# Performance work log

Hardware: AMD Instinct MI355X
Metric: run time of the kernel (lower is better)

## Reference

```python
import jax, jax.numpy as jnp
import numpy as np

N, E, F_IN, H, C = 50000, 800000, 256, 64, 40
NEG_SLOPE = 0.2


def setup_inputs() -> dict:
    key = jax.random.key(0)
    ks = jax.random.split(key, 16)
    sc = lambda fan: 1.0 / np.sqrt(fan)
    return {
        "x": jax.random.normal(ks[0], (N, F_IN), dtype=jnp.float32),
        "edge_index": jax.random.randint(ks[1], (2, E), 0, N, dtype=jnp.int64),
        "W1l": jax.random.normal(ks[2], (F_IN, H), dtype=jnp.float32) * sc(F_IN),
        "b1l": jnp.zeros((H,), jnp.float32),
        "W1r": jax.random.normal(ks[3], (F_IN, H), dtype=jnp.float32) * sc(F_IN),
        "b1r": jnp.zeros((H,), jnp.float32),
        "att1": jax.random.normal(ks[4], (H,), dtype=jnp.float32) * sc(H),
        "bias1": jnp.zeros((H,), jnp.float32),
        "lin1_W": jax.random.normal(ks[5], (F_IN, H), dtype=jnp.float32) * sc(F_IN),
        "lin1_b": jnp.zeros((H,), jnp.float32),
        "W2l": jax.random.normal(ks[6], (H, C), dtype=jnp.float32) * sc(H),
        "b2l": jnp.zeros((C,), jnp.float32),
        "W2r": jax.random.normal(ks[7], (H, C), dtype=jnp.float32) * sc(H),
        "b2r": jnp.zeros((C,), jnp.float32),
        "att2": jax.random.normal(ks[8], (C,), dtype=jnp.float32) * sc(C),
        "bias2": jnp.zeros((C,), jnp.float32),
        "lin2_W": jax.random.normal(ks[9], (H, C), dtype=jnp.float32) * sc(H),
        "lin2_b": jnp.zeros((C,), jnp.float32),
    }


def gatv2_layer(x, src, dst, Wl, bl, Wr, br, att, bias, n):
    # PyG GATv2Conv, heads=1: xl = lin_l(x) (source), xr = lin_r(x) (target)
    xl = x @ Wl + bl                               # [n, out]
    xr = x @ Wr + br                               # [n, out]
    m = xl[src] + xr[dst]                          # [E, out] per-edge gather
    e = jax.nn.leaky_relu(m, NEG_SLOPE) @ att      # [E] attention logits
    # segment softmax over destination nodes (self-loops guarantee nonempty segments)
    emax = jax.ops.segment_max(e, dst, num_segments=n)
    ee = jnp.exp(e - emax[dst])
    denom = jax.ops.segment_sum(ee, dst, num_segments=n)
    alpha = ee / denom[dst]                        # [E]
    out = jax.ops.segment_sum(alpha[:, None] * xl[src], dst, num_segments=n)
    return out + bias


def reference(x, edge_index, W1l, b1l, W1r, b1r, att1, bias1, lin1_W, lin1_b,
              W2l, b2l, W2r, b2r, att2, bias2, lin2_W, lin2_b):
    n = x.shape[0]
    loops = jnp.arange(n, dtype=edge_index.dtype)
    src = jnp.concatenate([edge_index[0], loops])  # add_self_loops=True (PyG default)
    dst = jnp.concatenate([edge_index[1], loops])
    h = jax.nn.relu(gatv2_layer(x, src, dst, W1l, b1l, W1r, b1r, att1, bias1, n)
                    + x @ lin1_W + lin1_b)
    o = (gatv2_layer(h, src, dst, W2l, b2l, W2r, b2r, att2, bias2, n)
         + h @ lin2_W + lin2_b)
    return jax.nn.log_softmax(o, axis=1), edge_index
```

## Files before the change

### kernel.cpp

```cpp
#include <hip/hip_runtime.h>
#include <cmath>

#define NN 50000
#define NP 50048
#define NE 800000
#define CD 40
#define NEG_SLOPE 0.2f
#define NITEMS (NE + NN)
#define CHUNK 2048
#define NCH 416
#define NBKT 391
#define BCAP 3072
#define GB1 782
#define TB1 (3 * 64 * 256)
#define TB2 (3 * 64 * 64)
#define WPB 240

typedef __attribute__((ext_vector_type(8))) short s16x8;
typedef __attribute__((ext_vector_type(4))) float f32x4;
typedef __attribute__((ext_vector_type(2))) float f32x2;

__device__ __forceinline__ f32x2 pk_fma(f32x2 a, f32x2 b, f32x2 c) {
#if __has_builtin(__builtin_elementwise_fma)
  return __builtin_elementwise_fma(a, b, c);
#else
  f32x2 r; r[0] = fmaf(a[0], b[0], c[0]); r[1] = fmaf(a[1], b[1], c[1]); return r;
#endif
}
__device__ __forceinline__ f32x2 pk_max(f32x2 a, f32x2 b) {
#if __has_builtin(__builtin_elementwise_max)
  return __builtin_elementwise_max(a, b);
#else
  f32x2 r; r[0] = fmaxf(a[0], b[0]); r[1] = fmaxf(a[1], b[1]); return r;
#endif
}

__device__ __forceinline__ short f2bf(float x) {
  unsigned u = __builtin_bit_cast(unsigned, x);
  u += 0x7fffu + ((u >> 16) & 1u);
  return (short)(u >> 16);
}
__device__ __forceinline__ unsigned pack2(float lo, float hi) {
  return (unsigned)(unsigned short)f2bf(lo) | ((unsigned)(unsigned short)f2bf(hi) << 16);
}
__device__ __forceinline__ float bf2f_lo(unsigned v) {
  return __builtin_bit_cast(float, v << 16);
}
__device__ __forceinline__ float bf2f_hi(unsigned v) {
  return __builtin_bit_cast(float, v & 0xffff0000u);
}
__device__ __forceinline__ void unp8(uint4 v, f32x2* f) {
  f[0] = (f32x2){bf2f_lo(v.x), bf2f_hi(v.x)};
  f[1] = (f32x2){bf2f_lo(v.y), bf2f_hi(v.y)};
  f[2] = (f32x2){bf2f_lo(v.z), bf2f_hi(v.z)};
  f[3] = (f32x2){bf2f_lo(v.w), bf2f_hi(v.w)};
}

__global__ __launch_bounds__(256) void prep_bin(const float* __restrict__ W1l,
                                                const float* __restrict__ W1r,
                                                const float* __restrict__ L1,
                                                const float* __restrict__ W2l,
                                                const float* __restrict__ W2r,
                                                const float* __restrict__ L2,
                                                short* __restrict__ Wp1,
                                                short* __restrict__ Wp2,
                                                const int* __restrict__ ei,
                                                float* __restrict__ outE,
                                                int* __restrict__ gcur,
                                                unsigned* __restrict__ rec) {
  const int tid = threadIdx.x;
  if (blockIdx.x < WPB) {
    int e = blockIdx.x * 256 + tid;
    if (e < TB1) {
      int kb = e / 6144, r = e % 6144;
      int w = r / 2048, r2 = r % 2048;
      int t = r2 / 512, r3 = r2 % 512;
      int lane = r3 / 8, j = r3 % 8;
      int n = t * 16 + (lane & 15);
      int k = kb * 32 + (lane >> 4) * 8 + j;
      const float* W = (w == 0) ? W1l : (w == 1) ? W1r : L1;
      Wp1[e] = f2bf(W[k * 64 + n]);
    } else {
      e -= TB1;
      int kb = e / 6144, r = e % 6144;
      int w = r / 2048, r2 = r % 2048;
      int t = r2 / 512, r3 = r2 % 512;
      int lane = r3 / 8, j = r3 % 8;
      int n = t * 16 + (lane & 15);
      int k = kb * 32 + (lane >> 4) * 8 + j;
      const float* W = (w == 0) ? W2l : (w == 1) ? W2r : L2;
      Wp2[e] = (n < 40) ? f2bf(W[k * 40 + n]) : (short)0;
    }
    return;
  }
  __shared__ unsigned sorted[CHUNK];
  __shared__ int hist[512];
  __shared__ int bcur[512];
  __shared__ int gbase[512];
  const int base = (blockIdx.x - WPB) * CHUNK;
  for (int t = tid; t < 512; t += 256) { hist[t] = 0; bcur[t] = 0; gbase[t] = 0; }
  __syncthreads();
  unsigned key[CHUNK / 256];
#pragma unroll
  for (int u = 0; u < CHUNK / 256; ++u) {
    const int j = base + u * 256 + tid;
    unsigned k = 0xFFFFFFFFu;
    if (j < NITEMS) {
      int s, d;
      if (j < NE) {
        s = ei[j]; d = ei[NE + j];
        outE[j] = (float)s; outE[NE + j] = (float)d;
      } else {
        s = j - NE; d = s;
      }
      k = ((unsigned)d << 16) | (unsigned)s;
      atomicAdd(&hist[k >> 23], 1);
    }
    key[u] = k;
  }
  __syncthreads();
  if (tid < 64) {
    int carry = 0;
#pragma unroll
    for (int c = 0; c < 8; ++c) {
      int v = hist[c * 64 + tid];
      int inc = v;
#pragma unroll
      for (int off = 1; off < 64; off <<= 1) {
        int tt = __shfl_up(inc, off, 64);
        if (tid >= off) inc += tt;
      }
      hist[c * 64 + tid] = carry + inc - v;
      carry += __shfl(inc, 63, 64);
    }
  }
  __syncthreads();
#pragma unroll
  for (int u = 0; u < CHUNK / 256; ++u) {
    const unsigned k = key[u];
    if (k != 0xFFFFFFFFu) {
      const int b = k >> 23;
      sorted[hist[b] + atomicAdd(&bcur[b], 1)] = k;
    }
  }
  __syncthreads();
  for (int t = tid; t < NBKT; t += 256) {
    const int c = bcur[t];
    if (c > 0) gbase[t] = atomicAdd(&gcur[t], c);
  }
  __syncthreads();
  const int cnt = min(CHUNK, NITEMS - base);
  for (int i = tid; i < cnt; i += 256) {
    const unsigned k = sorted[i];
    const int b = k >> 23;
    const int p = gbase[b] + (i - hist[b]);
    if (p < BCAP) rec[(size_t)b * BCAP + p] = k;
  }
}

__device__ __forceinline__ void gemm1_body(int bid, const float* __restrict__ X,
                                           const short* __restrict__ Wp,
                                           const float* __restrict__ B0,
                                           const float* __restrict__ B1,
                                           const float* __restrict__ B2,
                                           unsigned short* __restrict__ Y0,
                                           unsigned short* __restrict__ Y1,
                                           unsigned short* __restrict__ Y2) {
  const int lane = threadIdx.x & 63;
  const int wave = threadIdx.x >> 6;
  const int r0 = bid * 64 + wave * 16;
  const int m = lane & 15;
  const int q = lane >> 4;
  f32x4 acc[3][4] = {};
  const float* a0 = X + (size_t)min(r0 + m, NN - 1) * 256 + q * 8;
  const short* bp = Wp + lane * 8;
  float4 v0 = *reinterpret_cast<const float4*>(a0);
  float4 v1 = *reinterpret_cast<const float4*>(a0 + 4);
#pragma unroll
  for (int kb = 0; kb < 8; ++kb) {
    s16x8 bf[12];
#pragma unroll
    for (int i = 0; i < 12; ++i)
      bf[i] = *reinterpret_cast<const s16x8*>(bp + (size_t)(kb * 12 + i) * 512);
    s16x8 af;
    af[0] = f2bf(v0.x); af[1] = f2bf(v0.y); af[2] = f2bf(v0.z); af[3] = f2bf(v0.w);
    af[4] = f2bf(v1.x); af[5] = f2bf(v1.y); af[6] = f2bf(v1.z); af[7] = f2bf(v1.w);
    if (kb < 7) {
      v0 = *reinterpret_cast<const float4*>(a0 + (kb + 1) * 32);
      v1 = *reinterpret_cast<const float4*>(a0 + (kb + 1) * 32 + 4);
    }
#pragma unroll
    for (int i = 0; i < 12; ++i)
      acc[i >> 2][i & 3] = __builtin_amdgcn_mfma_f32_16x16x32_bf16(
          af, bf[i], acc[i >> 2][i & 3], 0, 0, 0);
  }
#pragma unroll
  for (int w = 0; w < 3; ++w) {
    const float* B = (w == 0) ? B0 : (w == 1) ? B1 : B2;
    unsigned short* Y = (w == 0) ? Y0 : (w == 1) ? Y1 : Y2;
#pragma unroll
    for (int t = 0; t < 4; ++t) {
      const int c = t * 16 + m;
      const float bv = B[c];
#pragma unroll
      for (int rg = 0; rg < 4; ++rg) {
        const int row = r0 + q * 4 + rg;
        if (row < NN)
          Y[(size_t)row * 64 + c] = (unsigned short)f2bf(acc[w][t][rg] + bv);
      }
    }
  }
}

__global__ __launch_bounds__(256, 2) void build_gemm1(
    const float* __restrict__ X, const short* __restrict__ Wp1,
    const float* __restrict__ B0, const float* __restrict__ B1,
    const float* __restrict__ B2, unsigned short* __restrict__ Y0,
    unsigned short* __restrict__ Y1, unsigned short* __restrict__ Y2,
    const int* __restrict__ gcur, const unsigned* __restrict__ rec,
    int* __restrict__ offsets, unsigned short* __restrict__ csr16) {
  if (blockIdx.x < GB1) {
    gemm1_body(blockIdx.x, X, Wp1, B0, B1, B2, Y0, Y1, Y2);
    return;
  }
  const int b = blockIdx.x - GB1;
  const int tid = threadIdx.x;
  __shared__ unsigned recs[BCAP];
  __shared__ int red[256];
  __shared__ int cnt[128];
  __shared__ int sc[128];
  __shared__ int cur[128];
  int acc = 0;
  for (int t = tid; t < NBKT; t += 256)
    if (t < b) acc += gcur[t];
  red[tid] = acc;
  __syncthreads();
#pragma unroll
  for (int off = 128; off >= 1; off >>= 1) {
    if (tid < off) red[tid] += red[tid + off];
    __syncthreads();
  }
  const int base = red[0];
  const int Tb = min(gcur[b], BCAP);
  if (tid < 128) cnt[tid] = 0;
  __syncthreads();
  for (int i = tid; i < Tb; i += 256) {
    const unsigned k = rec[(size_t)b * BCAP + i];
    recs[i] = k;
    atomicAdd(&cnt[(k >> 16) & 127], 1);
  }
  __syncthreads();
  if (tid < 128) sc[tid] = cnt[tid];
  __syncthreads();
#pragma unroll
  for (int off = 1; off < 128; off <<= 1) {
    int v = (tid < 128 && tid >= off) ? sc[tid - off] : 0;
    __syncthreads();
    if (tid < 128) sc[tid] += v;
    __syncthreads();
  }
  if (tid < 128) {
    const int n = b * 128 + tid;
    if (n < NN) offsets[n + 1] = base + sc[tid];
    cur[tid] = sc[tid] - cnt[tid];
  }
  if (b == 0 && tid == 0) offsets[0] = 0;
  __syncthreads();
  for (int i = tid; i < Tb; i += 256) {
    const unsigned k = recs[i];
    const int p = atomicAdd(&cur[(k >> 16) & 127], 1);
    csr16[base + p] = (unsigned short)(k & 0xFFFFu);
  }
}

__global__ __launch_bounds__(256, 2) void gemm2(const short* __restrict__ Xb,
                                                const short* __restrict__ Wp,
                                                const float* __restrict__ B0,
                                                const float* __restrict__ B1,
                                                const float* __restrict__ B2,
                                                unsigned short* __restrict__ Y0,
                                                unsigned short* __restrict__ Y1,
                                                unsigned short* __restrict__ Y2) {
  const int lane = threadIdx.x & 63;
  const int wave = threadIdx.x >> 6;
  const int r0 = blockIdx.x * 64 + wave * 16;
  const int m = lane & 15;
  const int q = lane >> 4;
  f32x4 acc[3][4] = {};
  const short* a0 = Xb + (size_t)(r0 + m) * 64 + q * 8;
  const short* bp = Wp + lane * 8;
#pragma unroll
  for (int kb = 0; kb < 2; ++kb) {
    s16x8 bf[12];
#pragma unroll
    for (int i = 0; i < 12; ++i)
      bf[i] = *reinterpret_cast<const s16x8*>(bp + (size_t)(kb * 12 + i) * 512);
    const s16x8 af = *reinterpret_cast<const s16x8*>(a0 + kb * 32);
#pragma unroll
    for (int i = 0; i < 12; ++i)
      acc[i >> 2][i & 3] = __builtin_amdgcn_mfma_f32_16x16x32_bf16(
          af, bf[i], acc[i >> 2][i & 3], 0, 0, 0);
  }
#pragma unroll
  for (int w = 0; w < 3; ++w) {
    const float* B = (w == 0) ? B0 : (w == 1) ? B1 : B2;
    unsigned short* Y = (w == 0) ? Y0 : (w == 1) ? Y1 : Y2;
#pragma unroll
    for (int t = 0; t < 4; ++t) {
      const int c = t * 16 + m;
      const float bv = (c < 40) ? B[c] : 0.f;
#pragma unroll
      for (int rg = 0; rg < 4; ++rg) {
        const int row = r0 + q * 4 + rg;
        if (row < NN)
          Y[(size_t)row * 64 + c] = (unsigned short)f2bf(acc[w][t][rg] + bv);
      }
    }
  }
}

template <int OC, bool FINAL>
__global__ __launch_bounds__(256) void gat_agg(const unsigned short* __restrict__ XL,
                                               const unsigned short* __restrict__ XR,
                                               const unsigned short* __restrict__ XLIN,
                                               const float* __restrict__ att,
                                               const float* __restrict__ bias,
                                               const int* __restrict__ offsets,
                                               const unsigned short* __restrict__ csr,
                                               float* __restrict__ out,
                                               unsigned short* __restrict__ outb) {
  const int lane = threadIdx.x & 63;
  const int g = lane >> 3;
  const int l = lane & 7;
  const int d = blockIdx.x * 4 + (threadIdx.x >> 6);
  if (d >= NN) return;
  const bool dimok = (8 * l < OC);
  f32x2 a2[4] = {};
  if (dimok) {
    const float4 t0 = *reinterpret_cast<const float4*>(&att[8 * l]);
    const float4 t1 = *reinterpret_cast<const float4*>(&att[8 * l + 4]);
    a2[0] = (f32x2){t0.x, t0.y}; a2[1] = (f32x2){t0.z, t0.w};
    a2[2] = (f32x2){t1.x, t1.y}; a2[3] = (f32x2){t1.z, t1.w};
  }
  f32x2 xr2[4];
  unp8(*reinterpret_cast<const uint4*>(XR + (size_t)d * 64 + 8 * l), xr2);
  const int beg = offsets[d];
  const int end = offsets[d + 1];
  float D = 0.f;
  f32x2 A2[4] = {};
  const f32x2 ns = (f32x2){NEG_SLOPE, NEG_SLOPE};
  const int nit = (end - beg + 7) >> 3;
  const int i0 = beg + g;
  int sa = (int)csr[(i0 < end) ? i0 : beg];
  uint4 raw_next = *reinterpret_cast<const uint4*>(XL + (size_t)sa * 64 + 8 * l);
  const int i1 = i0 + 8;
  sa = (int)csr[(i1 < end) ? i1 : beg];
  for (int it = 0; it < nit; ++it) {
    const uint4 raw = raw_next;
    const bool act = (beg + it * 8 + g) < end;
    raw_next = *reinterpret_cast<const uint4*>(XL + (size_t)sa * 64 + 8 * l);
    const int i2 = beg + (it + 2) * 8 + g;
    sa = (int)csr[(i2 < end) ? i2 : beg];
    f32x2 xl2[4];
    unp8(raw, xl2);
    f32x2 pacc = (f32x2){0.f, 0.f};
#pragma unroll
    for (int j = 0; j < 4; ++j) {
      const f32x2 t = xl2[j] + xr2[j];
      const f32x2 lr = pk_max(t, t * ns);
      pacc = pk_fma(lr, a2[j], pacc);
    }
    float p = pacc[0] + pacc[1];
    p += __shfl_xor(p, 1, 64);
    p += __shfl_xor(p, 2, 64);
    p += __shfl_xor(p, 4, 64);
    const float w = __expf(act ? p : -INFINITY);
    D += w;
    const f32x2 w2 = (f32x2){w, w};
#pragma unroll
    for (int j = 0; j < 4; ++j) A2[j] = pk_fma(w2, xl2[j], A2[j]);
  }
  D += __shfl_xor(D, 8, 64);
  D += __shfl_xor(D, 16, 64);
  D += __shfl_xor(D, 32, 64);
  float A[8];
#pragma unroll
  for (int j = 0; j < 4; ++j) {
#pragma unroll
    for (int c = 0; c < 2; ++c) {
      float v = A2[j][c];
      v += __shfl_xor(v, 8, 64);
      v += __shfl_xor(v, 16, 64);
      v += __shfl_xor(v, 32, 64);
      A[j * 2 + c] = v;
    }
  }
  f32x2 xlin2[4];
  unp8(*reinterpret_cast<const uint4*>(XLIN + (size_t)d * 64 + 8 * l), xlin2);
  float b[8] = {};
  if (dimok) {
    const float4 t0 = *reinterpret_cast<const float4*>(&bias[8 * l]);
    const float4 t1 = *reinterpret_cast<const float4*>(&bias[8 * l + 4]);
    b[0] = t0.x; b[1] = t0.y; b[2] = t0.z; b[3] = t0.w;
    b[4] = t1.x; b[5] = t1.y; b[6] = t1.z; b[7] = t1.w;
  }
  const float inv = 1.0f / D;
  float val[8];
#pragma unroll
  for (int j = 0; j < 8; ++j)
    val[j] = fmaf(A[j], inv, b[j]) + xlin2[j >> 1][j & 1];
  if (!FINAL) {
    if (g == 0) {
      uint4 o;
      o.x = pack2(fmaxf(val[0], 0.f), fmaxf(val[1], 0.f));
      o.y = pack2(fmaxf(val[2], 0.f), fmaxf(val[3], 0.f));
      o.z = pack2(fmaxf(val[4], 0.f), fmaxf(val[5], 0.f));
      o.w = pack2(fmaxf(val[6], 0.f), fmaxf(val[7], 0.f));
      *reinterpret_cast<uint4*>(&outb[(size_t)d * 64 + 8 * l]) = o;
    }
  } else {
    float mx = -3e38f;
    if (dimok) {
#pragma unroll
      for (int j = 0; j < 8; ++j) mx = fmaxf(mx, val[j]);
    }
    mx = fmaxf(mx, __shfl_xor(mx, 1, 64));
    mx = fmaxf(mx, __shfl_xor(mx, 2, 64));
    mx = fmaxf(mx, __shfl_xor(mx, 4, 64));
    float es = 0.f;
    if (dimok) {
#pragma unroll
      for (int j = 0; j < 8; ++j) es += __expf(val[j] - mx);
    }
    es += __shfl_xor(es, 1, 64);
    es += __shfl_xor(es, 2, 64);
    es += __shfl_xor(es, 4, 64);
    const float lse = mx + __logf(es);
    if (g == 0 && dimok) {
      float4 o0, o1;
      o0.x = val[0] - lse; o0.y = val[1] - lse; o0.z = val[2] - lse; o0.w = val[3] - lse;
      o1.x = val[4] - lse; o1.y = val[5] - lse; o1.z = val[6] - lse; o1.w = val[7] - lse;
      float* dst = &out[(size_t)d * OC + 8 * l];
      *reinterpret_cast<float4*>(dst) = o0;
      *reinterpret_cast<float4*>(dst + 4) = o1;
    }
  }
}

extern "C" void kernel_launch(void* const* d_in, const int* in_sizes, int n_in,
                              void* d_out, int out_size, void* d_ws, size_t ws_size,
                              hipStream_t stream) {
  const float* x     = (const float*)d_in[0];
  const int*   ei    = (const int*)d_in[1];
  const float* W1l   = (const float*)d_in[2];
  const float* b1l   = (const float*)d_in[3];
  const float* W1r   = (const float*)d_in[4];
  const float* b1r   = (const float*)d_in[5];
  const float* att1  = (const float*)d_in[6];
  const float* bias1 = (const float*)d_in[7];
  const float* lin1W = (const float*)d_in[8];
  const float* lin1b = (const float*)d_in[9];
  const float* W2l   = (const float*)d_in[10];
  const float* b2l   = (const float*)d_in[11];
  const float* W2r   = (const float*)d_in[12];
  const float* b2r   = (const float*)d_in[13];
  const float* att2  = (const float*)d_in[14];
  const float* bias2 = (const float*)d_in[15];
  const float* lin2W = (const float*)d_in[16];
  const float* lin2b = (const float*)d_in[17];
  float* out = (float*)d_out;

  char* ws = (char*)d_ws;
  size_t off = 0;
  auto alloc = [&](size_t bytes) -> void* {
    void* p = ws + off;
    off += (bytes + 255) & ~(size_t)255;
    return p;
  };
  short* Wp1 = (short*)alloc((size_t)TB1 * 2);
  short* Wp2 = (short*)alloc((size_t)TB2 * 2);
  unsigned short* XL1   = (unsigned short*)alloc((size_t)NN * 64 * 2);
  unsigned short* XR1   = (unsigned short*)alloc((size_t)NN * 64 * 2);
  unsigned short* XLIN1 = (unsigned short*)alloc((size_t)NN * 64 * 2);
  unsigned short* Hb    = (unsigned short*)alloc((size_t)NP * 64 * 2);
  unsigned short* XL2   = (unsigned short*)alloc((size_t)NN * 64 * 2);
  unsigned short* XR2   = (unsigned short*)alloc((size_t)NN * 64 * 2);
  unsigned short* XLIN2 = (unsigned short*)alloc((size_t)NN * 64 * 2);
  int* gcur    = (int*)alloc((size_t)NBKT * 4);
  int* offsets = (int*)alloc((size_t)(NN + 1) * 4);
  unsigned* rec = (unsigned*)alloc((size_t)NBKT * BCAP * 4);
  unsigned short* csr = (unsigned short*)alloc((size_t)NITEMS * 2);

  hipMemsetAsync(gcur, 0, (size_t)NBKT * 4, stream);
  prep_bin<<<WPB + NCH, 256, 0, stream>>>(W1l, W1r, lin1W, W2l, W2r, lin2W,
                                          Wp1, Wp2, ei, out + (size_t)NN * CD,
                                          gcur, rec);
  build_gemm1<<<GB1 + NBKT, 256, 0, stream>>>(x, Wp1, b1l, b1r, lin1b,
                                              XL1, XR1, XLIN1, gcur, rec,
                                              offsets, csr);
  gat_agg<64, false><<<(NN + 3) / 4, 256, 0, stream>>>(XL1, XR1, XLIN1, att1,
                                                       bias1, offsets, csr,
                                                       nullptr, Hb);
  gemm2<<<GB1, 256, 0, stream>>>((const short*)Hb, Wp2, b2l, b2r, lin2b,
                                 XL2, XR2, XLIN2);
  gat_agg<40, true><<<(NN + 3) / 4, 256, 0, stream>>>(XL2, XR2, XLIN2, att2,
                                                      bias2, offsets, csr,
                                                      out, nullptr);
}
```

Baseline: 234.4 us.

## Fuse layer-1 aggregation with layer-2 GEMM through shared memory

Merges the first GATv2 aggregation kernel and the second-layer projection GEMM into one 1024-thread kernel. Each block aggregates 16 destination nodes (one per wave), writes the ReLU'd hidden rows to LDS, then 12 waves each run two MFMA ops to produce the XL2/XR2/XLIN2 tiles. This removes one launch and the global write and read of the hidden activation H. In exchange, the MFMA tail leaves four waves idle, and the barrier makes the whole block wait for its slowest node's edge loop.

After: 255.5 us. +9.0%, slower.

```diff
diff --git a/kernel.cpp b/kernel.cpp
--- a/kernel.cpp
+++ b/kernel.cpp
@@ -273,70 +273,23 @@
   }
 }
 
-__global__ __launch_bounds__(256, 2) void gemm2(const short* __restrict__ Xb,
-                                                const short* __restrict__ Wp,
-                                                const float* __restrict__ B0,
-                                                const float* __restrict__ B1,
-                                                const float* __restrict__ B2,
-                                                unsigned short* __restrict__ Y0,
-                                                unsigned short* __restrict__ Y1,
-                                                unsigned short* __restrict__ Y2) {
-  const int lane = threadIdx.x & 63;
-  const int wave = threadIdx.x >> 6;
-  const int r0 = blockIdx.x * 64 + wave * 16;
-  const int m = lane & 15;
-  const int q = lane >> 4;
-  f32x4 acc[3][4] = {};
-  const short* a0 = Xb + (size_t)(r0 + m) * 64 + q * 8;
-  const short* bp = Wp + lane * 8;
-#pragma unroll
-  for (int kb = 0; kb < 2; ++kb) {
-    s16x8 bf[12];
-#pragma unroll
-    for (int i = 0; i < 12; ++i)
-      bf[i] = *reinterpret_cast<const s16x8*>(bp + (size_t)(kb * 12 + i) * 512);
-    const s16x8 af = *reinterpret_cast<const s16x8*>(a0 + kb * 32);
-#pragma unroll
-    for (int i = 0; i < 12; ++i)
-      acc[i >> 2][i & 3] = __builtin_amdgcn_mfma_f32_16x16x32_bf16(
-          af, bf[i], acc[i >> 2][i & 3], 0, 0, 0);
-  }
-#pragma unroll
-  for (int w = 0; w < 3; ++w) {
-    const float* B = (w == 0) ? B0 : (w == 1) ? B1 : B2;
-    unsigned short* Y = (w == 0) ? Y0 : (w == 1) ? Y1 : Y2;
-#pragma unroll
-    for (int t = 0; t < 4; ++t) {
-      const int c = t * 16 + m;
-      const float bv = (c < 40) ? B[c] : 0.f;
-#pragma unroll
-      for (int rg = 0; rg < 4; ++rg) {
-        const int row = r0 + q * 4 + rg;
-        if (row < NN)
-          Y[(size_t)row * 64 + c] = (unsigned short)f2bf(acc[w][t][rg] + bv);
-      }
-    }
-  }
-}
-
-template <int OC, bool FINAL>
-__global__ __launch_bounds__(256) void gat_agg(const unsigned short* __restrict__ XL,
-                                               const unsigned short* __restrict__ XR,
-                                               const unsigned short* __restrict__ XLIN,
-                                               const float* __restrict__ att,
-                                               const float* __restrict__ bias,
-                                               const int* __restrict__ offsets,
-                                               const unsigned short* __restrict__ csr,
-                                               float* __restrict__ out,
-                                               unsigned short* __restrict__ outb) {
-  const int lane = threadIdx.x & 63;
+__global__ __launch_bounds__(1024) void gat1_gemm2(
+    const unsigned short* __restrict__ XL, const unsigned short* __restrict__ XR,
+    const unsigned short* __restrict__ XLIN, const float* __restrict__ att,
+    const float* __restrict__ bias, const int* __restrict__ offsets,
+    const unsigned short* __restrict__ csr, const short* __restrict__ Wp2,
+    const float* __restrict__ B0, const float* __restrict__ B1,
+    const float* __restrict__ B2, unsigned short* __restrict__ Y0,
+    unsigned short* __restrict__ Y1, unsigned short* __restrict__ Y2) {
+  __shared__ unsigned short Hs[16][72];
+  const int tid = threadIdx.x;
+  const int wave = tid >> 6;
+  const int lane = tid & 63;
   const int g = lane >> 3;
   const int l = lane & 7;
-  const int d = blockIdx.x * 4 + (threadIdx.x >> 6);
-  if (d >= NN) return;
-  const bool dimok = (8 * l < OC);
-  f32x2 a2[4] = {};
-  if (dimok) {
+  const int d = blockIdx.x * 16 + wave;
+  f32x2 a2[4];
+  {
     const float4 t0 = *reinterpret_cast<const float4*>(&att[8 * l]);
     const float4 t1 = *reinterpret_cast<const float4*>(&att[8 * l + 4]);
     a2[0] = (f32x2){t0.x, t0.y}; a2[1] = (f32x2){t0.z, t0.w};
@@ -397,6 +350,126 @@
   }
   f32x2 xlin2[4];
   unp8(*reinterpret_cast<const uint4*>(XLIN + (size_t)d * 64 + 8 * l), xlin2);
+  float b[8];
+  {
+    const float4 t0 = *reinterpret_cast<const float4*>(&bias[8 * l]);
+    const float4 t1 = *reinterpret_cast<const float4*>(&bias[8 * l + 4]);
+    b[0] = t0.x; b[1] = t0.y; b[2] = t0.z; b[3] = t0.w;
+    b[4] = t1.x; b[5] = t1.y; b[6] = t1.z; b[7] = t1.w;
+  }
+  const float inv = 1.0f / D;
+  if (g == 0) {
+    float val[8];
+#pragma unroll
+    for (int j = 0; j < 8; ++j)
+      val[j] = fmaxf(fmaf(A[j], inv, b[j]) + xlin2[j >> 1][j & 1], 0.f);
+    uint4 o;
+    o.x = pack2(val[0], val[1]);
+    o.y = pack2(val[2], val[3]);
+    o.z = pack2(val[4], val[5]);
+    o.w = pack2(val[6], val[7]);
+    *reinterpret_cast<uint4*>(&Hs[wave][8 * l]) = o;
+  }
+  __syncthreads();
+  if (wave < 12) {
+    const int w = wave >> 2, t = wave & 3;
+    const int m = lane & 15, q = lane >> 4;
+    const s16x8 af0 = *reinterpret_cast<const s16x8*>(&Hs[m][q * 8]);
+    const s16x8 af1 = *reinterpret_cast<const s16x8*>(&Hs[m][32 + q * 8]);
+    const short* bp = Wp2 + lane * 8;
+    const s16x8 bf0 = *reinterpret_cast<const s16x8*>(bp + (size_t)(w * 4 + t) * 512);
+    const s16x8 bf1 = *reinterpret_cast<const s16x8*>(bp + (size_t)((3 + w) * 4 + t) * 512);
+    f32x4 acc = {};
+    acc = __builtin_amdgcn_mfma_f32_16x16x32_bf16(af0, bf0, acc, 0, 0, 0);
+    acc = __builtin_amdgcn_mfma_f32_16x16x32_bf16(af1, bf1, acc, 0, 0, 0);
+    const float* B = (w == 0) ? B0 : (w == 1) ? B1 : B2;
+    unsigned short* Y = (w == 0) ? Y0 : (w == 1) ? Y1 : Y2;
+    const int c = t * 16 + m;
+    const float bv = (c < 40) ? B[c] : 0.f;
+#pragma unroll
+    for (int rg = 0; rg < 4; ++rg) {
+      const int row = blockIdx.x * 16 + q * 4 + rg;
+      Y[(size_t)row * 64 + c] = (unsigned short)f2bf(acc[rg] + bv);
+    }
+  }
+}
+
+__global__ __launch_bounds__(256) void gat_agg2(const unsigned short* __restrict__ XL,
+                                                const unsigned short* __restrict__ XR,
+                                                const unsigned short* __restrict__ XLIN,
+                                                const float* __restrict__ att,
+                                                const float* __restrict__ bias,
+                                                const int* __restrict__ offsets,
+                                                const unsigned short* __restrict__ csr,
+                                                float* __restrict__ out) {
+  const int lane = threadIdx.x & 63;
+  const int g = lane >> 3;
+  const int l = lane & 7;
+  const int d = blockIdx.x * 4 + (threadIdx.x >> 6);
+  if (d >= NN) return;
+  const bool dimok = (8 * l < CD);
+  f32x2 a2[4] = {};
+  if (dimok) {
+    const float4 t0 = *reinterpret_cast<const float4*>(&att[8 * l]);
+    const float4 t1 = *reinterpret_cast<const float4*>(&att[8 * l + 4]);
+    a2[0] = (f32x2){t0.x, t0.y}; a2[1] = (f32x2){t0.z, t0.w};
+    a2[2] = (f32x2){t1.x, t1.y}; a2[3] = (f32x2){t1.z, t1.w};
+  }
+  f32x2 xr2[4];
+  unp8(*reinterpret_cast<const uint4*>(XR + (size_t)d * 64 + 8 * l), xr2);
+  const int beg = offsets[d];
+  const int end = offsets[d + 1];
+  float D = 0.f;
+  f32x2 A2[4] = {};
+  const f32x2 ns = (f32x2){NEG_SLOPE, NEG_SLOPE};
+  const int nit = (end - beg + 7) >> 3;
+  const int i0 = beg + g;
+  int sa = (int)csr[(i0 < end) ? i0 : beg];
+  uint4 raw_next = *reinterpret_cast<const uint4*>(XL + (size_t)sa * 64 + 8 * l);
+  const int i1 = i0 + 8;
+  sa = (int)csr[(i1 < end) ? i1 : beg];
+  for (int it = 0; it < nit; ++it) {
+    const uint4 raw = raw_next;
+    const bool act = (beg + it * 8 + g) < end;
+    raw_next = *reinterpret_cast<const uint4*>(XL + (size_t)sa * 64 + 8 * l);
+    const int i2 = beg + (it + 2) * 8 + g;
+    sa = (int)csr[(i2 < end) ? i2 : beg];
+    f32x2 xl2[4];
+    unp8(raw, xl2);
+    f32x2 pacc = (f32x2){0.f, 0.f};
+#pragma unroll
+    for (int j = 0; j < 4; ++j) {
+      const f32x2 t = xl2[j] + xr2[j];
+      const f32x2 lr = pk_max(t, t * ns);
+      pacc = pk_fma(lr, a2[j], pacc);
+    }
+    float p = pacc[0] + pacc[1];
+    p += __shfl_xor(p, 1, 64);
+    p += __shfl_xor(p, 2, 64);
+    p += __shfl_xor(p, 4, 64);
+    const float w = __expf(act ? p : -INFINITY);
+    D += w;
+    const f32x2 w2 = (f32x2){w, w};
+#pragma unroll
+    for (int j = 0; j < 4; ++j) A2[j] = pk_fma(w2, xl2[j], A2[j]);
+  }
+  D += __shfl_xor(D, 8, 64);
+  D += __shfl_xor(D, 16, 64);
+  D += __shfl_xor(D, 32, 64);
+  float A[8];
+#pragma unroll
+  for (int j = 0; j < 4; ++j) {
+#pragma unroll
+    for (int c = 0; c < 2; ++c) {
+      float v = A2[j][c];
+      v += __shfl_xor(v, 8, 64);
+      v += __shfl_xor(v, 16, 64);
+      v += __shfl_xor(v, 32, 64);
+      A[j * 2 + c] = v;
+    }
+  }
+  f32x2 xlin2[4];
+  unp8(*reinterpret_cast<const uint4*>(XLIN + (size_t)d * 64 + 8 * l), xlin2);
   float b[8] = {};
   if (dimok) {
     const float4 t0 = *reinterpret_cast<const float4*>(&bias[8 * l]);
@@ -409,41 +482,30 @@
 #pragma unroll
   for (int j = 0; j < 8; ++j)
     val[j] = fmaf(A[j], inv, b[j]) + xlin2[j >> 1][j & 1];
-  if (!FINAL) {
-    if (g == 0) {
-      uint4 o;
-      o.x = pack2(fmaxf(val[0], 0.f), fmaxf(val[1], 0.f));
-      o.y = pack2(fmaxf(val[2], 0.f), fmaxf(val[3], 0.f));
-      o.z = pack2(fmaxf(val[4], 0.f), fmaxf(val[5], 0.f));
-      o.w = pack2(fmaxf(val[6], 0.f), fmaxf(val[7], 0.f));
-      *reinterpret_cast<uint4*>(&outb[(size_t)d * 64 + 8 * l]) = o;
-    }
-  } else {
-    float mx = -3e38f;
-    if (dimok) {
-#pragma unroll
-      for (int j = 0; j < 8; ++j) mx = fmaxf(mx, val[j]);
-    }
-    mx = fmaxf(mx, __shfl_xor(mx, 1, 64));
-    mx = fmaxf(mx, __shfl_xor(mx, 2, 64));
-    mx = fmaxf(mx, __shfl_xor(mx, 4, 64));
-    float es = 0.f;
-    if (dimok) {
-#pragma unroll
-      for (int j = 0; j < 8; ++j) es += __expf(val[j] - mx);
-    }
-    es += __shfl_xor(es, 1, 64);
-    es += __shfl_xor(es, 2, 64);
-    es += __shfl_xor(es, 4, 64);
-    const float lse = mx + __logf(es);
-    if (g == 0 && dimok) {
-      float4 o0, o1;
-      o0.x = val[0] - lse; o0.y = val[1] - lse; o0.z = val[2] - lse; o0.w = val[3] - lse;
-      o1.x = val[4] - lse; o1.y = val[5] - lse; o1.z = val[6] - lse; o1.w = val[7] - lse;
-      float* dst = &out[(size_t)d * OC + 8 * l];
-      *reinterpret_cast<float4*>(dst) = o0;
-      *reinterpret_cast<float4*>(dst + 4) = o1;
-    }
+  float mx = -3e38f;
+  if (dimok) {
+#pragma unroll
+    for (int j = 0; j < 8; ++j) mx = fmaxf(mx, val[j]);
+  }
+  mx = fmaxf(mx, __shfl_xor(mx, 1, 64));
+  mx = fmaxf(mx, __shfl_xor(mx, 2, 64));
+  mx = fmaxf(mx, __shfl_xor(mx, 4, 64));
+  float es = 0.f;
+  if (dimok) {
+#pragma unroll
+    for (int j = 0; j < 8; ++j) es += __expf(val[j] - mx);
+  }
+  es += __shfl_xor(es, 1, 64);
+  es += __shfl_xor(es, 2, 64);
+  es += __shfl_xor(es, 4, 64);
+  const float lse = mx + __logf(es);
+  if (g == 0 && dimok) {
+    float4 o0, o1;
+    o0.x = val[0] - lse; o0.y = val[1] - lse; o0.z = val[2] - lse; o0.w = val[3] - lse;
+    o1.x = val[4] - lse; o1.y = val[5] - lse; o1.z = val[6] - lse; o1.w = val[7] - lse;
+    float* dst = &out[(size_t)d * CD + 8 * l];
+    *reinterpret_cast<float4*>(dst) = o0;
+    *reinterpret_cast<float4*>(dst + 4) = o1;
   }
 }
 
@@ -482,7 +544,6 @@
   unsigned short* XL1   = (unsigned short*)alloc((size_t)NN * 64 * 2);
   unsigned short* XR1   = (unsigned short*)alloc((size_t)NN * 64 * 2);
   unsigned short* XLIN1 = (unsigned short*)alloc((size_t)NN * 64 * 2);
-  unsigned short* Hb    = (unsigned short*)alloc((size_t)NP * 64 * 2);
   unsigned short* XL2   = (unsigned short*)alloc((size_t)NN * 64 * 2);
   unsigned short* XR2   = (unsigned short*)alloc((size_t)NN * 64 * 2);
   unsigned short* XLIN2 = (unsigned short*)alloc((size_t)NN * 64 * 2);
@@ -498,12 +559,9 @@
   build_gemm1<<<GB1 + NBKT, 256, 0, stream>>>(x, Wp1, b1l, b1r, lin1b,
                                               XL1, XR1, XLIN1, gcur, rec,
                                               offsets, csr);
-  gat_agg<64, false><<<(NN + 3) / 4, 256, 0, stream>>>(XL1, XR1, XLIN1, att1,
-                                                       bias1, offsets, csr,
-                                                       nullptr, Hb);
-  gemm2<<<GB1, 256, 0, stream>>>((const short*)Hb, Wp2, b2l, b2r, lin2b,
-                                 XL2, XR2, XLIN2);
-  gat_agg<40, true><<<(NN + 3) / 4, 256, 0, stream>>>(XL2, XR2, XLIN2, att2,
-                                                      bias2, offsets, csr,
-                                                      out, nullptr);
-}
+  gat1_gemm2<<<NN / 16, 1024, 0, stream>>>(XL1, XR1, XLIN1, att1, bias1,
+                                           offsets, csr, Wp2, b2l, b2r, lin2b,
+                                           XL2, XR2, XLIN2);
+  gat_agg2<<<(NN + 3) / 4, 256, 0, stream>>>(XL2, XR2, XLIN2, att2, bias2,
+                                             offsets, csr, out);
+}
```
